# Kernel tuning notes

Hardware: AMD Instinct MI355X
Metric: run time of the kernel (lower is better)

## Reference

```python
import jax, jax.numpy as jnp
import numpy as np

B, T, D_IN, D, OUT, L, NDAYS = 32, 2048, 512, 256, 41, 3, 45
INNER = 2 * D  # expand=2

def silu(x):
    return x * jax.nn.sigmoid(x)

def layernorm(x, s, b, eps=1e-5):
    m = x.mean(-1, keepdims=True)
    v = ((x - m) ** 2).mean(-1, keepdims=True)
    return (x - m) / jnp.sqrt(v + eps) * s + b

def dwconv(x, k, b):
    # x: [B,T,C], k: [C,4] depthwise kernel, b: [C]
    # torch Conv1d(padding=2)[..., :T] == pad (left=2, right=1), valid window 4
    y = jax.lax.conv_general_dilated(
        x.transpose(0, 2, 1), k[:, None, :], window_strides=(1,),
        padding=[(2, 1)], feature_group_count=k.shape[0],
        dimension_numbers=('NCH', 'OIH', 'NCH'))
    return y.transpose(0, 2, 1) + b

def soft_window(x, Win, convK, convB, dtW, dtB, Wout):
    # x: [B,T,D]
    xz = x @ Win                      # [B,T,2*INNER]
    xi, z = jnp.split(xz, 2, axis=-1)
    xc = silu(dwconv(xi, convK, convB))
    dt = jax.nn.softplus(xc @ dtW + dtB)
    w = jnp.exp(-jnp.cumsum(dt, axis=1) * 0.1)
    return (xc * w * silu(z)) @ Wout  # [B,T,D]

def setup_inputs() -> dict:
    key = jax.random.key(0)
    ks = iter(jax.random.split(key, 40))
    n = lambda shp, s=0.02: jax.random.normal(next(ks), shp, dtype=jnp.float32) * s
    inp = {}
    inp['x'] = jax.random.normal(next(ks), (B, T, D_IN), dtype=jnp.float32)
    inp['day_ids'] = jax.random.randint(next(ks), (B,), 0, NDAYS)
    inp['adapter_W'] = jnp.tile(jnp.eye(D_IN)[None], (NDAYS, 1, 1)) + n((NDAYS, D_IN, D_IN))
    inp['adapter_b'] = n((NDAYS, D_IN))
    inp['cW1'] = n((D_IN, D)); inp['cb1'] = n((D,))
    inp['cln1_s'] = jnp.ones((D,)); inp['cln1_b'] = jnp.zeros((D,))
    inp['cW2'] = n((D, D)); inp['cb2'] = n((D,))
    inp['cln2_s'] = jnp.ones((D,)); inp['cln2_b'] = jnp.zeros((D,))
    # mamba params: leading dims [L, 2] for (fwd, bwd) directions
    inp['m_in'] = n((L, 2, D, 2 * INNER))
    inp['m_convK'] = n((L, 2, INNER, 4), 0.2); inp['m_convB'] = n((L, 2, INNER))
    inp['m_dtW'] = n((L, 2, INNER, INNER)); inp['m_dtB'] = n((L, 2, INNER))
    inp['m_out'] = n((L, 2, INNER, D))
    inp['proj_W'] = n((L, 2 * D, D)); inp['proj_b'] = n((L, D))
    inp['norm_s'] = jnp.ones((L, D)); inp['norm_b'] = jnp.zeros((L, D))
    inp['outW'] = n((D, OUT)); inp['outb'] = n((OUT,))
    return inp

def reference(x, day_ids, adapter_W, adapter_b, cW1, cb1, cln1_s, cln1_b,
              cW2, cb2, cln2_s, cln2_b, m_in, m_convK, m_convB, m_dtW, m_dtB,
              m_out, proj_W, proj_b, norm_s, norm_b, outW, outb):
    # Day adapter: batched gather-matmul (replaces per-sample python loop)
    h = jnp.einsum('btd,bde->bte', x, adapter_W[day_ids]) + adapter_b[day_ids][:, None, :]
    h = jax.nn.soft_sign(h)
    # input compress MLP (dropout = eval identity)
    h = silu(layernorm(h @ cW1 + cb1, cln1_s, cln1_b))
    h = silu(layernorm(h @ cW2 + cb2, cln2_s, cln2_b))
    # stacked bidirectional pseudo-SSM layers
    for l in range(L):
        fwd = soft_window(h, m_in[l, 0], m_convK[l, 0], m_convB[l, 0],
                          m_dtW[l, 0], m_dtB[l, 0], m_out[l, 0])
        hr = h[:, ::-1, :]
        bwd = soft_window(hr, m_in[l, 1], m_convK[l, 1], m_convB[l, 1],
                          m_dtW[l, 1], m_dtB[l, 1], m_out[l, 1])[:, ::-1, :]
        combined = jnp.concatenate([fwd, bwd], axis=-1) @ proj_W[l] + proj_b[l]
        h = layernorm(h + combined, norm_s[l], norm_b[l])
    return jax.nn.log_softmax(h @ outW + outb, axis=-1)
```

## Files before the change

kernel.cpp:

```cpp
#include <hip/hip_runtime.h>
#include <hip/hip_bf16.h>
#include <cstdint>
#include <math.h>

typedef __bf16 bf16_t;
typedef bf16_t bf16x8 __attribute__((ext_vector_type(8)));
typedef float f32x4 __attribute__((ext_vector_type(4)));

#define B_ 32
#define T_ 2048
#define D_ 256
#define INNER_ 512
#define L_ 3
#define CHUNK_ 64
#define NCHUNK_ (T_/CHUNK_)

typedef const __attribute__((address_space(1))) void* gas_t;
typedef __attribute__((address_space(3))) void* las_t;
__device__ __forceinline__ void gll16(const void* g, void* l) {
  __builtin_amdgcn_global_load_lds((gas_t)g, (las_t)l, 16, 0, 0);
}

struct GemmP {
  const bf16_t* A;
  const bf16_t* Bt;
  const float* bias;
  float* outF;
  bf16_t* outB;
  const int* day_ids;
  long bStrideBt;
  int bStrideBias;
  int K, N, ldout, colOff, act, revA, revC, nValid;
};

__global__ __launch_bounds__(256, 4)
void gemm_kernel(GemmP p) {
  __shared__ bf16_t As[2*128*32];
  __shared__ bf16_t Bs[2*128*32];
  const int tid = threadIdx.x;
  const int wave = tid >> 6, lane = tid & 63;
  const int m0 = blockIdx.x << 7, n0 = blockIdx.y << 7;
  const bf16_t* Bt = p.Bt;
  const float* bias = p.bias;
  if (p.day_ids) {
    int day = p.day_ids[m0 >> 11];
    Bt += (long)day * p.bStrideBt;
    if (bias) bias += (long)day * p.bStrideBias;
  }
  const int K = p.K;
  const int srow = tid >> 2;
  const int sc = ((tid & 3) - (tid >> 4)) & 3;
  const int sk = sc << 3;

  int ar0 = m0 + srow, ar1 = m0 + srow + 64;
  if (p.revA) {
    int t0 = ar0 & (T_-1); ar0 = ar0 - t0 + (T_-1 - t0);
    int t1 = ar1 & (T_-1); ar1 = ar1 - t1 + (T_-1 - t1);
  }
  const bf16_t* aP0 = p.A + (long)ar0 * K + sk;
  const bf16_t* aP1 = p.A + (long)ar1 * K + sk;
  const bf16_t* bP0 = Bt + (long)(n0 + srow) * K + sk;
  const bf16_t* bP1 = bP0 + (long)64 * K;

  char* aL = (char*)As + wave * 1024;
  char* bL = (char*)Bs + wave * 1024;

  f32x4 acc[4][4] = {};
  const int mw = ((wave >> 1) << 6), nw = ((wave & 1) << 6);
  const int fr = lane & 15;
  const int foff = (((lane >> 4) + (fr >> 2)) & 3) << 4;

  gll16(aP0, aL);
  gll16(aP1, aL + 4096);
  gll16(bP0, bL);
  gll16(bP1, bL + 4096);
  __syncthreads();

  const int nIter = K >> 5;
  for (int it = 0; it < nIter; ++it) {
    const int cur = (it & 1) << 13;
    const int nxt = cur ^ 8192;
    if (it + 1 < nIter) {
      const int k1 = (it + 1) << 5;
      gll16(aP0 + k1, aL + nxt);
      gll16(aP1 + k1, aL + nxt + 4096);
      gll16(bP0 + k1, bL + nxt);
      gll16(bP1 + k1, bL + nxt + 4096);
    }
    bf16x8 af[4], bfr[4];
#pragma unroll
    for (int i = 0; i < 4; i++)
      af[i] = *(const bf16x8*)((char*)As + cur + (mw + i*16 + fr)*64 + foff);
#pragma unroll
    for (int j = 0; j < 4; j++)
      bfr[j] = *(const bf16x8*)((char*)Bs + cur + (nw + j*16 + fr)*64 + foff);
#pragma unroll
    for (int i = 0; i < 4; i++)
#pragma unroll
      for (int j = 0; j < 4; j++)
        acc[i][j] = __builtin_amdgcn_mfma_f32_16x16x32_bf16(af[i], bfr[j], acc[i][j], 0, 0, 0);
    __syncthreads();
  }

  const int cn = lane & 15, rq = (lane >> 4) << 2;
#pragma unroll
  for (int i = 0; i < 4; i++) {
#pragma unroll
    for (int r = 0; r < 4; r++) {
      int gr = m0 + mw + i*16 + rq + r;
      int orow = gr;
      if (p.revC) { int t = gr & (T_-1); orow = gr - t + (T_-1 - t); }
      long rowOff = (long)orow * p.ldout + p.colOff;
#pragma unroll
      for (int j = 0; j < 4; j++) {
        int col = n0 + nw + j*16 + cn;
        if (col >= p.nValid) continue;
        float v = acc[i][j][r];
        if (bias) v += bias[col];
        if (p.act == 1) {
          v = v / (1.f + fabsf(v));
        } else if (p.act == 2) {
          float e = __expf(-fabsf(v));
          v = fmaxf(v, 0.f) + __logf(1.f + e);
        }
        if (p.outF) p.outF[rowOff + col] = v;
        if (p.outB) p.outB[rowOff + col] = (bf16_t)v;
      }
    }
  }
}

__global__ __launch_bounds__(256)
void ln_kernel(const float* in, const bf16_t* resid, const float* s, const float* bb,
               bf16_t* outB, int doSilu) {
  int row = (blockIdx.x << 2) + (threadIdx.x >> 6);
  int lane = threadIdx.x & 63;
  long base = (long)row * D_ + (lane << 2);
  f32x4 v = *(const f32x4*)(in + base);
  if (resid) {
#pragma unroll
    for (int k = 0; k < 4; k++) v[k] += (float)resid[base + k];
  }
  float s1 = v[0] + v[1] + v[2] + v[3];
  float s2 = v[0]*v[0] + v[1]*v[1] + v[2]*v[2] + v[3]*v[3];
#pragma unroll
  for (int off = 1; off < 64; off <<= 1) {
    s1 += __shfl_xor(s1, off);
    s2 += __shfl_xor(s2, off);
  }
  float mean = s1 * (1.f / D_);
  float var = s2 * (1.f / D_) - mean * mean;
  float inv = rsqrtf(var + 1e-5f);
  f32x4 sv = *(const f32x4*)(s + (lane << 2));
  f32x4 bv = *(const f32x4*)(bb + (lane << 2));
#pragma unroll
  for (int k = 0; k < 4; k++) {
    float val = (v[k] - mean) * inv * sv[k] + bv[k];
    if (doSilu) val = val / (1.f + __expf(-val));
    outB[base + k] = (bf16_t)val;
  }
}

__global__ __launch_bounds__(256)
void conv_kernel(const bf16_t* xz, const float* K4, const float* cb, bf16_t* xc) {
  long idx = (long)blockIdx.x * 256 + threadIdx.x;
  int ch0 = ((int)(idx & 63)) << 3;
  long bt = idx >> 6;
  int t = (int)(bt & (T_-1));
  const bf16_t* base = xz + bt * (2*INNER_) + ch0;
  bf16x8 r0, r1, r2, r3;
  r2 = *(const bf16x8*)(base);
#pragma unroll
  for (int k = 0; k < 8; k++) { r0[k] = (bf16_t)0.f; r1[k] = (bf16_t)0.f; r3[k] = (bf16_t)0.f; }
  if (t >= 2) r0 = *(const bf16x8*)(base - 2*(2*INNER_));
  if (t >= 1) r1 = *(const bf16x8*)(base - (2*INNER_));
  if (t < T_-1) r3 = *(const bf16x8*)(base + (2*INNER_));
  bf16x8 o8;
#pragma unroll
  for (int k = 0; k < 8; k++) {
    f32x4 kk = *(const f32x4*)(K4 + ((ch0 + k) << 2));
    float a = cb[ch0 + k] + (float)r0[k]*kk[0] + (float)r1[k]*kk[1]
            + (float)r2[k]*kk[2] + (float)r3[k]*kk[3];
    o8[k] = (bf16_t)(a / (1.f + __expf(-a)));
  }
  *(bf16x8*)(xc + bt * INNER_ + ch0) = o8;
}

__global__ __launch_bounds__(256)
void chunksum_kernel(const bf16_t* dt, float* sums) {
  int bc = blockIdx.x * 4 + (threadIdx.x >> 6);
  int ch0 = (threadIdx.x & 63) << 3;
  const bf16_t* p = dt + (long)bc * CHUNK_ * INNER_ + ch0;
  float a[8] = {};
  for (int i = 0; i < CHUNK_; i++) {
    bf16x8 v = *(const bf16x8*)(p + (long)i * INNER_);
#pragma unroll
    for (int k = 0; k < 8; k++) a[k] += (float)v[k];
  }
  float* o = sums + (long)bc * INNER_ + ch0;
#pragma unroll
  for (int k = 0; k < 8; k++) o[k] = a[k];
}

__global__ __launch_bounds__(256)
void y_kernel(const bf16_t* dt, const bf16_t* xz, bf16_t* xc, const float* sums) {
  int bc = blockIdx.x * 4 + (threadIdx.x >> 6);
  int b = bc >> 5;
  int c = bc & 31;
  int ch0 = (threadIdx.x & 63) << 3;
  float acc[8] = {};
  const float* sp = sums + (long)b * NCHUNK_ * INNER_ + ch0;
  for (int cp = 0; cp < c; cp++) {
#pragma unroll
    for (int k = 0; k < 8; k++) acc[k] += sp[(long)cp * INNER_ + k];
  }
  long bt0 = (long)bc * CHUNK_;
  for (int i = 0; i < CHUNK_; i++) {
    long bt = bt0 + i;
    bf16x8 d8 = *(const bf16x8*)(dt + bt * INNER_ + ch0);
    bf16x8 z8 = *(const bf16x8*)(xz + bt * (2*INNER_) + INNER_ + ch0);
    bf16x8 x8 = *(const bf16x8*)(xc + bt * INNER_ + ch0);
    bf16x8 o8;
#pragma unroll
    for (int k = 0; k < 8; k++) {
      acc[k] += (float)d8[k];
      float w = __expf(-0.1f * acc[k]);
      float zz = (float)z8[k];
      float sz = zz / (1.f + __expf(-zz));
      o8[k] = (bf16_t)((float)x8[k] * w * sz);
    }
    *(bf16x8*)(xc + bt * INNER_ + ch0) = o8;
  }
}

__global__ __launch_bounds__(256)
void lsm_kernel(const float* logits, float* out) {
  int row = (blockIdx.x << 2) + (threadIdx.x >> 6);
  int lane = threadIdx.x & 63;
  float v = (lane < 41) ? logits[(long)row * 41 + lane] : -3.4e38f;
  float m = v;
#pragma unroll
  for (int off = 1; off < 64; off <<= 1) m = fmaxf(m, __shfl_xor(m, off));
  float e = (lane < 41) ? __expf(v - m) : 0.f;
  float ssum = e;
#pragma unroll
  for (int off = 1; off < 64; off <<= 1) ssum += __shfl_xor(ssum, off);
  float ls = __logf(ssum);
  if (lane < 41) out[(long)row * 41 + lane] = v - m - ls;
}

__global__ void tconv_kernel(const float* in, bf16_t* out, int R, int C) {
  __shared__ float tile[32][33];
  const float* ip = in + (long)blockIdx.z * R * C;
  bf16_t* op = out + (long)blockIdx.z * R * C;
  int c0 = blockIdx.x << 5, r0 = blockIdx.y << 5;
  int tx = threadIdx.x, ty = threadIdx.y;
  for (int i = ty; i < 32; i += 8) {
    int r = r0 + i, c = c0 + tx;
    tile[i][tx] = (r < R && c < C) ? ip[(long)r * C + c] : 0.f;
  }
  __syncthreads();
  for (int i = ty; i < 32; i += 8) {
    int c = c0 + i, r = r0 + tx;
    if (c < C && r < R) op[(long)c * R + r] = (bf16_t)tile[tx][i];
  }
}

__global__ void cvt_kernel(const float* in, bf16_t* out, long n) {
  long i = ((long)blockIdx.x * blockDim.x + threadIdx.x) << 3;
  if (i >= n) return;
  f32x4 a = *(const f32x4*)(in + i);
  f32x4 b = *(const f32x4*)(in + i + 4);
  bf16x8 o;
#pragma unroll
  for (int k = 0; k < 4; k++) { o[k] = (bf16_t)a[k]; o[k+4] = (bf16_t)b[k]; }
  *(bf16x8*)(out + i) = o;
}

__global__ void zfill_kernel(bf16_t* p, int n) {
  int i = blockIdx.x * 256 + threadIdx.x;
  if (i < n) p[i] = (bf16_t)0.f;
}

extern "C" void kernel_launch(void* const* d_in, const int* in_sizes, int n_in,
                              void* d_out, int out_size, void* d_ws, size_t ws_size,
                              hipStream_t stream) {
  (void)in_sizes; (void)n_in; (void)out_size;
  const float* x         = (const float*)d_in[0];
  const int*   day_ids   = (const int*)d_in[1];
  const float* adapter_W = (const float*)d_in[2];
  const float* adapter_b = (const float*)d_in[3];
  const float* cW1       = (const float*)d_in[4];
  const float* cb1       = (const float*)d_in[5];
  const float* cln1_s    = (const float*)d_in[6];
  const float* cln1_b    = (const float*)d_in[7];
  const float* cW2       = (const float*)d_in[8];
  const float* cb2       = (const float*)d_in[9];
  const float* cln2_s    = (const float*)d_in[10];
  const float* cln2_b    = (const float*)d_in[11];
  const float* m_in      = (const float*)d_in[12];
  const float* m_convK   = (const float*)d_in[13];
  const float* m_convB   = (const float*)d_in[14];
  const float* m_dtW     = (const float*)d_in[15];
  const float* m_dtB     = (const float*)d_in[16];
  const float* m_out     = (const float*)d_in[17];
  const float* proj_W    = (const float*)d_in[18];
  const float* proj_b    = (const float*)d_in[19];
  const float* norm_s    = (const float*)d_in[20];
  const float* norm_b    = (const float*)d_in[21];
  const float* outW      = (const float*)d_in[22];
  const float* outb      = (const float*)d_in[23];
  float* out = (float*)d_out;

  char* ws = (char*)d_ws;
  size_t off = 0;
  auto alloc = [&](size_t bytes) -> char* {
    char* p = ws + off;
    off += (bytes + 255) & ~(size_t)255;
    return p;
  };
  bf16_t* adapterT = (bf16_t*)alloc((size_t)45*512*512*2);
  bf16_t* cW1T     = (bf16_t*)alloc((size_t)256*512*2);
  bf16_t* cW2T     = (bf16_t*)alloc((size_t)256*256*2);
  bf16_t* m_inT    = (bf16_t*)alloc((size_t)6*1024*256*2);
  bf16_t* m_dtWT   = (bf16_t*)alloc((size_t)6*512*512*2);
  bf16_t* m_outT   = (bf16_t*)alloc((size_t)6*256*512*2);
  bf16_t* projT    = (bf16_t*)alloc((size_t)3*256*512*2);
  bf16_t* outWT    = (bf16_t*)alloc((size_t)128*256*2);

  int Bg = 0;
  {
    const int cands[6] = {32, 16, 8, 4, 2, 1};
    for (int ci = 0; ci < 6; ci++) {
      int c = cands[ci];
      size_t Mg = (size_t)c * T_;
      size_t need = Mg*2048 + 3*(Mg*1024) + Mg*512 + (size_t)c*NCHUNK_*INNER_*4
                    + 8*256;
      if (off + need <= ws_size) { Bg = c; break; }
    }
  }
  if (Bg == 0) return;
  const size_t Mg = (size_t)Bg * T_;
  char*  xzR  = alloc(Mg * 2048);
  char*  xcR  = alloc(Mg * 1024);
  char*  dtR  = alloc(Mg * 1024);
  char*  swR  = alloc(Mg * 1024);
  bf16_t* hG  = (bf16_t*)alloc(Mg * 512);
  float* sums = (float*)alloc((size_t)Bg * NCHUNK_ * INNER_ * 4);

  zfill_kernel<<<128, 256, 0, stream>>>(outWT, 128*256);
  dim3 tb(32, 8);
  tconv_kernel<<<dim3(16,16,45), tb, 0, stream>>>(adapter_W, adapterT, 512, 512);
  tconv_kernel<<<dim3(8,16,1),  tb, 0, stream>>>(cW1,  cW1T,  512, 256);
  tconv_kernel<<<dim3(8,8,1),   tb, 0, stream>>>(cW2,  cW2T,  256, 256);
  tconv_kernel<<<dim3(32,8,6),  tb, 0, stream>>>(m_in, m_inT, 256, 1024);
  tconv_kernel<<<dim3(16,16,6), tb, 0, stream>>>(m_dtW, m_dtWT, 512, 512);
  tconv_kernel<<<dim3(8,16,6),  tb, 0, stream>>>(m_out, m_outT, 512, 256);
  tconv_kernel<<<dim3(8,16,3),  tb, 0, stream>>>(proj_W, projT, 512, 256);
  tconv_kernel<<<dim3(2,8,1),   tb, 0, stream>>>(outW, outWT, 256, 41);

  auto gemm = [&](const bf16_t* A, const bf16_t* Bt, const float* bias,
                  float* outF, bf16_t* outB, int K, int N, int ldout, int colOff,
                  int act, int revA, int revC, const int* days, long bsBt, int bsBias,
                  int nValid) {
    GemmP p;
    p.A = A; p.Bt = Bt; p.bias = bias; p.outF = outF; p.outB = outB;
    p.day_ids = days; p.bStrideBt = bsBt; p.bStrideBias = bsBias;
    p.K = K; p.N = N; p.ldout = ldout; p.colOff = colOff;
    p.act = act; p.revA = revA; p.revC = revC; p.nValid = nValid;
    gemm_kernel<<<dim3((unsigned)(Mg/128), N/128), 256, 0, stream>>>(p);
  };

  for (int b0 = 0; b0 < B_; b0 += Bg) {
    const float* xg = x + (size_t)b0 * T_ * 512;

    bf16_t* x_bf = (bf16_t*)xzR;
    cvt_kernel<<<(unsigned)(Mg/4), 256, 0, stream>>>(xg, x_bf, (long)Mg*512);

    bf16_t* h0 = (bf16_t*)xcR;
    gemm(x_bf, adapterT, adapter_b, nullptr, h0, 512, 512, 512, 0, 1, 0, 0,
         day_ids + b0, (long)512*512, 512, 512);

    float* tmpF = (float*)dtR;
    gemm(h0, cW1T, cb1, tmpF, nullptr, 512, 256, 256, 0, 0, 0, 0, nullptr, 0, 0, 256);
    bf16_t* h1 = (bf16_t*)swR;
    ln_kernel<<<(unsigned)(Mg/4), 256, 0, stream>>>(tmpF, nullptr, cln1_s, cln1_b, h1, 1);

    gemm(h1, cW2T, cb2, tmpF, nullptr, 256, 256, 256, 0, 0, 0, 0, nullptr, 0, 0, 256);
    ln_kernel<<<(unsigned)(Mg/4), 256, 0, stream>>>(tmpF, nullptr, cln2_s, cln2_b, hG, 1);

    bf16_t* xz    = (bf16_t*)xzR;
    bf16_t* xc    = (bf16_t*)xcR;
    bf16_t* dt    = (bf16_t*)dtR;
    bf16_t* swcat = (bf16_t*)swR;

    for (int l = 0; l < L_; l++) {
      for (int dir = 0; dir < 2; dir++) {
        int ld = l*2 + dir;
        gemm(hG, m_inT + (size_t)ld*1024*256, nullptr, nullptr, xz,
             256, 1024, 1024, 0, 0, dir, 0, nullptr, 0, 0, 1024);
        conv_kernel<<<(unsigned)(Mg/4), 256, 0, stream>>>(
            xz, m_convK + (size_t)ld*512*4, m_convB + (size_t)ld*512, xc);
        gemm(xc, m_dtWT + (size_t)ld*512*512, m_dtB + (size_t)ld*512, nullptr, dt,
             512, 512, 512, 0, 2, 0, 0, nullptr, 0, 0, 512);
        chunksum_kernel<<<(unsigned)(Bg*8), 256, 0, stream>>>(dt, sums);
        y_kernel<<<(unsigned)(Bg*8), 256, 0, stream>>>(dt, xz, xc, sums);
        gemm(xc, m_outT + (size_t)ld*256*512, nullptr, nullptr, swcat,
             512, 256, 512, dir*256, 0, 0, dir, nullptr, 0, 0, 256);
      }
      float* tmpF2 = (float*)dtR;
      gemm(swcat, projT + (size_t)l*256*512, proj_b + (size_t)l*256, tmpF2, nullptr,
           512, 256, 256, 0, 0, 0, 0, nullptr, 0, 0, 256);
      ln_kernel<<<(unsigned)(Mg/4), 256, 0, stream>>>(tmpF2, hG, norm_s + (size_t)l*256,
                                                      norm_b + (size_t)l*256, hG, 0);
    }

    float* logits = (float*)xzR;
    gemm(hG, outWT, outb, logits, nullptr, 256, 128, 41, 0, 0, 0, 0,
         nullptr, 0, 0, 41);
    lsm_kernel<<<(unsigned)(Mg/4), 256, 0, stream>>>(logits, out + (size_t)b0 * T_ * 41);
  }
}
```

Measured before the change: 2.879 ms.

## Remap GEMM tiles for XCD locality and store pre-LN GEMM outputs as bf16

The GEMM launch becomes a 1D grid, with tile indices remapped so consecutive block IDs (round-robined across the 8 XCDs) fall on contiguous M ranges. This keeps A/B reuse within each XCD's L2. GEMM outputs feeding layernorm are now written as bf16 instead of fp32, and ln_kernel reads and writes them with vectorized bf16x4 accesses, halving that intermediate traffic. The trade-off is slightly lower precision before layernorm, and the remap assumes power-of-two tile counts divisible by 8.

```diff
diff --git a/kernel.cpp b/kernel.cpp
--- a/kernel.cpp
+++ b/kernel.cpp
@@ -5,6 +5,7 @@
 
 typedef __bf16 bf16_t;
 typedef bf16_t bf16x8 __attribute__((ext_vector_type(8)));
+typedef bf16_t bf16x4 __attribute__((ext_vector_type(4)));
 typedef float f32x4 __attribute__((ext_vector_type(4)));
 
 #define B_ 32
@@ -39,7 +40,15 @@
   __shared__ bf16_t Bs[2*128*32];
   const int tid = threadIdx.x;
   const int wave = tid >> 6, lane = tid & 63;
-  const int m0 = blockIdx.x << 7, n0 = blockIdx.y << 7;
+
+  const int nb = p.N >> 7;
+  const int nbs = __builtin_ctz(nb);
+  const int c8 = blockIdx.x & 7;
+  const int k8 = blockIdx.x >> 3;
+  const int mGrp = (gridDim.x >> 3) >> nbs;
+  const int m0 = (c8 * mGrp + (k8 >> nbs)) << 7;
+  const int n0 = (k8 & (nb - 1)) << 7;
+
   const bf16_t* Bt = p.Bt;
   const float* bias = p.bias;
   if (p.day_ids) {
@@ -131,15 +140,19 @@
 }
 
 __global__ __launch_bounds__(256)
-void ln_kernel(const float* in, const bf16_t* resid, const float* s, const float* bb,
+void ln_kernel(const bf16_t* in, const bf16_t* resid, const float* s, const float* bb,
                bf16_t* outB, int doSilu) {
   int row = (blockIdx.x << 2) + (threadIdx.x >> 6);
   int lane = threadIdx.x & 63;
   long base = (long)row * D_ + (lane << 2);
-  f32x4 v = *(const f32x4*)(in + base);
+  bf16x4 iv = *(const bf16x4*)(in + base);
+  float v[4];
+#pragma unroll
+  for (int k = 0; k < 4; k++) v[k] = (float)iv[k];
   if (resid) {
-#pragma unroll
-    for (int k = 0; k < 4; k++) v[k] += (float)resid[base + k];
+    bf16x4 rv = *(const bf16x4*)(resid + base);
+#pragma unroll
+    for (int k = 0; k < 4; k++) v[k] += (float)rv[k];
   }
   float s1 = v[0] + v[1] + v[2] + v[3];
   float s2 = v[0]*v[0] + v[1]*v[1] + v[2]*v[2] + v[3]*v[3];
@@ -153,12 +166,14 @@
   float inv = rsqrtf(var + 1e-5f);
   f32x4 sv = *(const f32x4*)(s + (lane << 2));
   f32x4 bv = *(const f32x4*)(bb + (lane << 2));
+  bf16x4 ov;
 #pragma unroll
   for (int k = 0; k < 4; k++) {
     float val = (v[k] - mean) * inv * sv[k] + bv[k];
     if (doSilu) val = val / (1.f + __expf(-val));
-    outB[base + k] = (bf16_t)val;
-  }
+    ov[k] = (bf16_t)val;
+  }
+  *(bf16x4*)(outB + base) = ov;
 }
 
 __global__ __launch_bounds__(256)
@@ -368,7 +383,7 @@
     p.day_ids = days; p.bStrideBt = bsBt; p.bStrideBias = bsBias;
     p.K = K; p.N = N; p.ldout = ldout; p.colOff = colOff;
     p.act = act; p.revA = revA; p.revC = revC; p.nValid = nValid;
-    gemm_kernel<<<dim3((unsigned)(Mg/128), N/128), 256, 0, stream>>>(p);
+    gemm_kernel<<<dim3((unsigned)((Mg/128) * (N/128))), 256, 0, stream>>>(p);
   };
 
   for (int b0 = 0; b0 < B_; b0 += Bg) {
@@ -381,13 +396,13 @@
     gemm(x_bf, adapterT, adapter_b, nullptr, h0, 512, 512, 512, 0, 1, 0, 0,
          day_ids + b0, (long)512*512, 512, 512);
 
-    float* tmpF = (float*)dtR;
-    gemm(h0, cW1T, cb1, tmpF, nullptr, 512, 256, 256, 0, 0, 0, 0, nullptr, 0, 0, 256);
+    bf16_t* tmpB = (bf16_t*)dtR;
+    gemm(h0, cW1T, cb1, nullptr, tmpB, 512, 256, 256, 0, 0, 0, 0, nullptr, 0, 0, 256);
     bf16_t* h1 = (bf16_t*)swR;
-    ln_kernel<<<(unsigned)(Mg/4), 256, 0, stream>>>(tmpF, nullptr, cln1_s, cln1_b, h1, 1);
-
-    gemm(h1, cW2T, cb2, tmpF, nullptr, 256, 256, 256, 0, 0, 0, 0, nullptr, 0, 0, 256);
-    ln_kernel<<<(unsigned)(Mg/4), 256, 0, stream>>>(tmpF, nullptr, cln2_s, cln2_b, hG, 1);
+    ln_kernel<<<(unsigned)(Mg/4), 256, 0, stream>>>(tmpB, nullptr, cln1_s, cln1_b, h1, 1);
+
+    gemm(h1, cW2T, cb2, nullptr, tmpB, 256, 256, 256, 0, 0, 0, 0, nullptr, 0, 0, 256);
+    ln_kernel<<<(unsigned)(Mg/4), 256, 0, stream>>>(tmpB, nullptr, cln2_s, cln2_b, hG, 1);
 
     bf16_t* xz    = (bf16_t*)xzR;
     bf16_t* xc    = (bf16_t*)xcR;
@@ -408,10 +423,10 @@
         gemm(xc, m_outT + (size_t)ld*256*512, nullptr, nullptr, swcat,
              512, 256, 512, dir*256, 0, 0, dir, nullptr, 0, 0, 256);
       }
-      float* tmpF2 = (float*)dtR;
-      gemm(swcat, projT + (size_t)l*256*512, proj_b + (size_t)l*256, tmpF2, nullptr,
+      bf16_t* tmpB2 = (bf16_t*)dtR;
+      gemm(swcat, projT + (size_t)l*256*512, proj_b + (size_t)l*256, nullptr, tmpB2,
            512, 256, 256, 0, 0, 0, 0, nullptr, 0, 0, 256);
-      ln_kernel<<<(unsigned)(Mg/4), 256, 0, stream>>>(tmpF2, hG, norm_s + (size_t)l*256,
+      ln_kernel<<<(unsigned)(Mg/4), 256, 0, stream>>>(tmpB2, hG, norm_s + (size_t)l*256,
                                                       norm_b + (size_t)l*256, hG, 0);
     }
 
```

After: 2.731 ms. 1.05x faster.
